# Performance work log

Hardware: AMD Instinct MI355X
Metric: run time of the kernel (lower is better)

Reference implementation:

```python
import jax, jax.numpy as jnp
import numpy as np

L, B, D_IN, D_LAT = 4096, 32, 128, 512

def setup_inputs() -> dict:
    key = jax.random.key(0)
    k1, k2, k3, k4 = jax.random.split(key, 4)
    X = jax.random.normal(k1, (L, B, D_IN), dtype=jnp.float32)
    h = jnp.zeros((B, D_LAT), dtype=jnp.float32)
    wx = jax.random.normal(k2, (D_IN, D_LAT), dtype=jnp.float32)
    wh = jax.random.normal(k3, (D_LAT,), dtype=jnp.float32)
    bh = jax.random.normal(k4, (D_LAT,), dtype=jnp.float32)
    return {"X": X, "h": h, "wx": wx, "wh": wh, "bh": bh}

def reference(X, h, wx, wh, bh):
    # Precompute the input projection for all timesteps (batched matmul outside the scan).
    # U: [L, B, latent]
    U = jnp.einsum('lbi,ij->lbj', X, wx) + bh
    # Linear diagonal recurrence: h_t = h_{t-1} * wh + U_t  (no activation inside loop,
    # matching the torch source which applies tanh only to the collected outputs).
    def step(h_prev, u_t):
        h_t = h_prev * wh + u_t
        return h_t, h_t
    _, hs = jax.lax.scan(step, h, U)  # hs: [L, B, latent]
    return jnp.tanh(hs)
```

## Files before the change

kernel.cpp:

```cpp
#include <hip/hip_runtime.h>
#include <cstdint>
#include <cstddef>

#define L_SEQ 4096
#define BATCH 32
#define DIN 128
#define DLAT 512
#define CHUNK 32
#define NCHUNK (L_SEQ / CHUNK)
#define USTRIDE 522

typedef __attribute__((ext_vector_type(8))) short short8;
typedef __attribute__((ext_vector_type(4))) float f32x4;

__device__ __forceinline__ unsigned short bf16rne(float x) {
    unsigned int b = __builtin_bit_cast(unsigned int, x);
    unsigned int r = b + 0x7FFFu + ((b >> 16) & 1u);
    return (unsigned short)(r >> 16);
}
__device__ __forceinline__ float bf16tof(unsigned short h) {
    return __builtin_bit_cast(float, (unsigned int)h << 16);
}
__device__ __forceinline__ void bf16split3(float x, unsigned short& h,
                                           unsigned short& m, unsigned short& l) {
    h = bf16rne(x);
    float r1 = x - bf16tof(h);
    m = bf16rne(r1);
    float r2 = r1 - bf16tof(m);
    l = bf16rne(r2);
}
__device__ __forceinline__ float pow32(float x) {
    float t = x;
    t = t * t; t = t * t; t = t * t; t = t * t; t = t * t;
    return t;
}

__global__ __launch_bounds__(256) void wx_transform(
    const float* __restrict__ wx,
    unsigned short* __restrict__ wxtH,
    unsigned short* __restrict__ wxtM,
    unsigned short* __restrict__ wxtL)
{
    const int gid  = blockIdx.x * 256 + threadIdx.x;
    const int fid  = gid >> 6;
    const int lane = gid & 63;
    const int kt = fid >> 5, nt = fid & 31;
    const int n  = nt * 16 + (lane & 15);
    const int kb = kt * 32 + (lane >> 4) * 8;

    short8 h8, m8, l8;
#pragma unroll
    for (int i = 0; i < 8; ++i) {
        unsigned short h, m, l;
        bf16split3(wx[(size_t)(kb + i) * DLAT + n], h, m, l);
        h8[i] = (short)h; m8[i] = (short)m; l8[i] = (short)l;
    }
    ((short8*)wxtH)[fid * 64 + lane] = h8;
    ((short8*)wxtM)[fid * 64 + lane] = m8;
    ((short8*)wxtL)[fid * 64 + lane] = l8;
}

__global__ __launch_bounds__(256) void rnn_local_mfma2(
    const float* __restrict__ X,
    const unsigned short* __restrict__ wxtH,
    const unsigned short* __restrict__ wxtM,
    const unsigned short* __restrict__ wxtL,
    const float* __restrict__ wh,
    const float* __restrict__ bh,
    float* __restrict__ out,
    float* __restrict__ F)
{
    __shared__ __align__(16) char smem[16 * 3 * 64 * 8 * 2];
    unsigned short* AF = (unsigned short*)smem;
    float* U = (float*)smem;

    const int tid  = threadIdx.x;
    const int c0 = blockIdx.x * 2, b = blockIdx.y;
    const int wid = tid >> 6, lane = tid & 63;

#pragma unroll
    for (int sl = 0; sl < 4; ++sl) {
        const int slot = tid + sl * 256;
        const int f  = slot >> 6;
        const int ls = slot & 63;
        const int cl = f >> 3, m = (f >> 2) & 1, kt = f & 3;
        const int t  = (c0 + cl) * CHUNK + m * 16 + (ls & 15);
        const int kb = kt * 32 + (ls >> 4) * 8;
        const float* p = X + ((size_t)t * BATCH + b) * DIN + kb;
        const float4 va = *(const float4*)p;
        const float4 vb = *(const float4*)(p + 4);
        float v[8] = {va.x, va.y, va.z, va.w, vb.x, vb.y, vb.z, vb.w};
        short8 h8, m8, l8;
#pragma unroll
        for (int i = 0; i < 8; ++i) {
            unsigned short h, mm, l;
            bf16split3(v[i], h, mm, l);
            h8[i] = (short)h; m8[i] = (short)mm; l8[i] = (short)l;
        }
        ((short8*)AF)[(f * 3 + 0) * 64 + ls] = h8;
        ((short8*)AF)[(f * 3 + 1) * 64 + ls] = m8;
        ((short8*)AF)[(f * 3 + 2) * 64 + ls] = l8;
    }
    __syncthreads();

    f32x4 acc[4][8];
#pragma unroll
    for (int tt = 0; tt < 4; ++tt)
#pragma unroll
        for (int j = 0; j < 8; ++j)
            acc[tt][j] = (f32x4){0.f, 0.f, 0.f, 0.f};

    const short8* AFv = (const short8*)AF;
    const short8* BHp = (const short8*)wxtH;
    const short8* BMp = (const short8*)wxtM;
    const short8* BLp = (const short8*)wxtL;

#pragma unroll
    for (int kt = 0; kt < 4; ++kt) {
        short8 ah[4], am[4], al[4];
#pragma unroll
        for (int tt = 0; tt < 4; ++tt) {
            const int f = tt * 4 + kt;
            ah[tt] = AFv[(f * 3 + 0) * 64 + lane];
            am[tt] = AFv[(f * 3 + 1) * 64 + lane];
            al[tt] = AFv[(f * 3 + 2) * 64 + lane];
        }
#pragma unroll
        for (int j = 0; j < 8; ++j) {
            const int idx = (kt * 32 + wid * 8 + j) * 64 + lane;
            const short8 bh8 = BHp[idx];
            const short8 bm8 = BMp[idx];
            const short8 bl8 = BLp[idx];
#pragma unroll
            for (int tt = 0; tt < 4; ++tt) {
                acc[tt][j] = __builtin_amdgcn_mfma_f32_16x16x32_bf16(am[tt], bm8, acc[tt][j], 0, 0, 0);
                acc[tt][j] = __builtin_amdgcn_mfma_f32_16x16x32_bf16(al[tt], bh8, acc[tt][j], 0, 0, 0);
                acc[tt][j] = __builtin_amdgcn_mfma_f32_16x16x32_bf16(ah[tt], bl8, acc[tt][j], 0, 0, 0);
                acc[tt][j] = __builtin_amdgcn_mfma_f32_16x16x32_bf16(am[tt], bh8, acc[tt][j], 0, 0, 0);
                acc[tt][j] = __builtin_amdgcn_mfma_f32_16x16x32_bf16(ah[tt], bm8, acc[tt][j], 0, 0, 0);
                acc[tt][j] = __builtin_amdgcn_mfma_f32_16x16x32_bf16(ah[tt], bh8, acc[tt][j], 0, 0, 0);
            }
        }
    }

    const int ch = tid * 2;
    const float2 whv = *(const float2*)(wh + ch);
    const float2 bhv = *(const float2*)(bh + ch);
    float l0 = 0.f, l1 = 0.f;

#pragma unroll
    for (int mm = 0; mm < 4; ++mm) {
        const int cl = mm >> 1, m = mm & 1;
        __syncthreads();
#pragma unroll
        for (int j = 0; j < 8; ++j) {
            const int col = wid * 128 + j * 16 + (lane & 15);
#pragma unroll
            for (int r4 = 0; r4 < 4; ++r4)
                U[((lane >> 4) * 4 + r4) * USTRIDE + col] = acc[mm][j][r4];
        }
        __syncthreads();
        for (int tl = 0; tl < 16; ++tl) {
            const float2 u = *(const float2*)&U[tl * USTRIDE + ch];
            l0 = fmaf(l0, whv.x, u.x + bhv.x);
            l1 = fmaf(l1, whv.y, u.y + bhv.y);
            const int t = (c0 + cl) * CHUNK + m * 16 + tl;
            float2 o; o.x = l0; o.y = l1;
            *(float2*)(out + ((size_t)t * BATCH + b) * DLAT + ch) = o;
        }
        if (m == 1) {
            float2 fo; fo.x = l0; fo.y = l1;
            *(float2*)(F + ((size_t)(c0 + cl) * BATCH + b) * DLAT + ch) = fo;
            l0 = 0.f; l1 = 0.f;
        }
    }
}

__global__ __launch_bounds__(128) void rnn_prefix(
    const float* __restrict__ h0, const float* __restrict__ wh,
    const float* __restrict__ F, float* __restrict__ Hpre)
{
    const int b  = blockIdx.x;
    const int j4 = threadIdx.x * 4;
    const size_t cb = (size_t)b * DLAT + j4;
    float4 w4 = *(const float4*)(wh + j4);
    float wv[4] = {w4.x, w4.y, w4.z, w4.w};
    float wc[4];
#pragma unroll
    for (int k = 0; k < 4; ++k) wc[k] = pow32(wv[k]);
    float4 h4 = *(const float4*)(h0 + cb);
    float Hv[4] = {h4.x, h4.y, h4.z, h4.w};
    for (int cg = 0; cg < NCHUNK / 4; ++cg) {
        float4 Fv[4];
#pragma unroll
        for (int i = 0; i < 4; ++i)
            Fv[i] = *(const float4*)(F + (size_t)(cg * 4 + i) * (BATCH * DLAT) + cb);
#pragma unroll
        for (int i = 0; i < 4; ++i) {
            float4 o = {Hv[0], Hv[1], Hv[2], Hv[3]};
            *(float4*)(Hpre + (size_t)(cg * 4 + i) * (BATCH * DLAT) + cb) = o;
            Hv[0] = fmaf(Hv[0], wc[0], Fv[i].x);
            Hv[1] = fmaf(Hv[1], wc[1], Fv[i].y);
            Hv[2] = fmaf(Hv[2], wc[2], Fv[i].z);
            Hv[3] = fmaf(Hv[3], wc[3], Fv[i].w);
        }
    }
}

__global__ __launch_bounds__(256) void rnn_fix2(
    const float* __restrict__ wh, const float* __restrict__ Hpre,
    float* __restrict__ out)
{
    const int tid = threadIdx.x;
    const int c   = blockIdx.x * 2 + (tid >> 7);
    const int b   = blockIdx.y;
    const int j4  = (tid & 127) * 4;
    const size_t cb = (size_t)b * DLAT + j4;
    float4 w4 = *(const float4*)(wh + j4);
    float4 H4 = *(const float4*)(Hpre + (size_t)c * (BATCH * DLAT) + cb);
    float wv[4] = {w4.x, w4.y, w4.z, w4.w};
    float Hv[4] = {H4.x, H4.y, H4.z, H4.w};
    float sc[4] = {wv[0], wv[1], wv[2], wv[3]};
#pragma unroll 4
    for (int d = 0; d < CHUNK; ++d) {
        const size_t off = ((size_t)(c * CHUNK + d) * BATCH + b) * DLAT + j4;
        float4 l4 = *(const float4*)(out + off);
        float4 res;
        res.x = tanhf(fmaf(sc[0], Hv[0], l4.x));
        res.y = tanhf(fmaf(sc[1], Hv[1], l4.y));
        res.z = tanhf(fmaf(sc[2], Hv[2], l4.z));
        res.w = tanhf(fmaf(sc[3], Hv[3], l4.w));
        *(float4*)(out + off) = res;
        sc[0] *= wv[0]; sc[1] *= wv[1]; sc[2] *= wv[2]; sc[3] *= wv[3];
    }
}

__global__ __launch_bounds__(256) void rnn_fix(
    const float* __restrict__ h0, const float* __restrict__ wh,
    const float* __restrict__ F, float* __restrict__ out)
{
    const int tid = threadIdx.x;
    const int c   = blockIdx.x * 2 + (tid >> 7);
    const int b   = blockIdx.y;
    const int j4  = (tid & 127) * 4;
    const size_t cb = (size_t)b * DLAT + j4;
    float4 h4 = *(const float4*)(h0 + cb);
    float4 w4 = *(const float4*)(wh + j4);
    float Hv[4] = {h4.x, h4.y, h4.z, h4.w};
    float wv[4] = {w4.x, w4.y, w4.z, w4.w};
    float wc[4];
#pragma unroll
    for (int k = 0; k < 4; ++k) wc[k] = pow32(wv[k]);
    for (int cc = 0; cc < c; ++cc) {
        const float4 Fv = *(const float4*)(F + ((size_t)cc * BATCH + b) * DLAT + j4);
        Hv[0] = fmaf(Hv[0], wc[0], Fv.x);
        Hv[1] = fmaf(Hv[1], wc[1], Fv.y);
        Hv[2] = fmaf(Hv[2], wc[2], Fv.z);
        Hv[3] = fmaf(Hv[3], wc[3], Fv.w);
    }
    float sc[4] = {wv[0], wv[1], wv[2], wv[3]};
    for (int d = 0; d < CHUNK; ++d) {
        const size_t off = ((size_t)(c * CHUNK + d) * BATCH + b) * DLAT + j4;
        float4 l4 = *(const float4*)(out + off);
        float4 res;
        res.x = tanhf(fmaf(sc[0], Hv[0], l4.x));
        res.y = tanhf(fmaf(sc[1], Hv[1], l4.y));
        res.z = tanhf(fmaf(sc[2], Hv[2], l4.z));
        res.w = tanhf(fmaf(sc[3], Hv[3], l4.w));
        *(float4*)(out + off) = res;
        sc[0] *= wv[0]; sc[1] *= wv[1]; sc[2] *= wv[2]; sc[3] *= wv[3];
    }
}

extern "C" void kernel_launch(void* const* d_in, const int* in_sizes, int n_in,
                              void* d_out, int out_size, void* d_ws, size_t ws_size,
                              hipStream_t stream) {
    const float* X  = (const float*)d_in[0];
    const float* h0 = (const float*)d_in[1];
    const float* wx = (const float*)d_in[2];
    const float* wh = (const float*)d_in[3];
    const float* bh = (const float*)d_in[4];
    float* out = (float*)d_out;

    const size_t seg = (size_t)NCHUNK * BATCH * DLAT;
    const size_t wxt_elems = 4 * 32 * 64 * 8;
    float* F = (float*)d_ws;
    unsigned short* wxtH = (unsigned short*)(F + seg);
    unsigned short* wxtM = wxtH + wxt_elems;
    unsigned short* wxtL = wxtM + wxt_elems;
    float* Hpre = (float*)(wxtL + wxt_elems);

    const size_t need_mid  = seg * 4 + wxt_elems * 3 * 2;
    const size_t need_full = need_mid + seg * 4;

    wx_transform<<<dim3(32), dim3(256), 0, stream>>>(wx, wxtH, wxtM, wxtL);
    rnn_local_mfma2<<<dim3(NCHUNK / 2, BATCH), dim3(256), 0, stream>>>(
        X, wxtH, wxtM, wxtL, wh, bh, out, F);
    if (ws_size >= need_full) {
        rnn_prefix<<<dim3(BATCH), dim3(128), 0, stream>>>(h0, wh, F, Hpre);
        rnn_fix2<<<dim3(NCHUNK / 2, BATCH), dim3(256), 0, stream>>>(wh, Hpre, out);
    } else {
        rnn_fix<<<dim3(NCHUNK / 2, BATCH), dim3(256), 0, stream>>>(h0, wh, F, out);
    }
}
```

Before: 233.1 us.

## Compute in-chunk scan in registers via cross-lane bpermute, one chunk per block

The local kernel now handles one 32-step chunk per block instead of two, which doubles the grid and halves the accumulator registers. The in-chunk linear recurrence is computed directly on the MFMA accumulator layout. Each lane does a 4-step serial scan, then a cross-lane prefix over 16-row groups using ds_bpermute with powers of wh. This removes the LDS round-trip of U, the __syncthreads barriers and the 16-step serial loop per thread. The cost is extra multiplies by wh powers, which can change floating-point rounding, and output stores now scatter across four timestep rows per lane.

```diff
diff --git a/kernel.cpp b/kernel.cpp
--- a/kernel.cpp
+++ b/kernel.cpp
@@ -8,7 +8,6 @@
 #define DLAT 512
 #define CHUNK 32
 #define NCHUNK (L_SEQ / CHUNK)
-#define USTRIDE 522
 
 typedef __attribute__((ext_vector_type(8))) short short8;
 typedef __attribute__((ext_vector_type(4))) float f32x4;
@@ -34,6 +33,10 @@
     t = t * t; t = t * t; t = t * t; t = t * t; t = t * t;
     return t;
 }
+__device__ __forceinline__ float bpermf(int idxb, float v) {
+    return __builtin_bit_cast(float,
+        __builtin_amdgcn_ds_bpermute(idxb, __builtin_bit_cast(int, v)));
+}
 
 __global__ __launch_bounds__(256) void wx_transform(
     const float* __restrict__ wx,
@@ -60,7 +63,7 @@
     ((short8*)wxtL)[fid * 64 + lane] = l8;
 }
 
-__global__ __launch_bounds__(256) void rnn_local_mfma2(
+__global__ __launch_bounds__(256) void rnn_local_mfma3(
     const float* __restrict__ X,
     const unsigned short* __restrict__ wxtH,
     const unsigned short* __restrict__ wxtM,
@@ -70,21 +73,21 @@
     float* __restrict__ out,
     float* __restrict__ F)
 {
-    __shared__ __align__(16) char smem[16 * 3 * 64 * 8 * 2];
-    unsigned short* AF = (unsigned short*)smem;
-    float* U = (float*)smem;
+    __shared__ __align__(16) unsigned short AF[8 * 3 * 64 * 8];
 
     const int tid  = threadIdx.x;
-    const int c0 = blockIdx.x * 2, b = blockIdx.y;
+    const int c = blockIdx.x, b = blockIdx.y;
     const int wid = tid >> 6, lane = tid & 63;
-
-#pragma unroll
-    for (int sl = 0; sl < 4; ++sl) {
+    const int g = lane >> 4;
+    const int col = lane & 15;
+
+#pragma unroll
+    for (int sl = 0; sl < 2; ++sl) {
         const int slot = tid + sl * 256;
         const int f  = slot >> 6;
         const int ls = slot & 63;
-        const int cl = f >> 3, m = (f >> 2) & 1, kt = f & 3;
-        const int t  = (c0 + cl) * CHUNK + m * 16 + (ls & 15);
+        const int mS = f >> 2, kt = f & 3;
+        const int t  = c * CHUNK + mS * 16 + (ls & 15);
         const int kb = kt * 32 + (ls >> 4) * 8;
         const float* p = X + ((size_t)t * BATCH + b) * DIN + kb;
         const float4 va = *(const float4*)p;
@@ -101,14 +104,22 @@
         ((short8*)AF)[(f * 3 + 1) * 64 + ls] = m8;
         ((short8*)AF)[(f * 3 + 2) * 64 + ls] = l8;
     }
+
+    float whj[8], bhj[8];
+#pragma unroll
+    for (int j = 0; j < 8; ++j) {
+        const int chj = wid * 128 + j * 16 + col;
+        whj[j] = wh[chj];
+        bhj[j] = bh[chj];
+    }
     __syncthreads();
 
-    f32x4 acc[4][8];
-#pragma unroll
-    for (int tt = 0; tt < 4; ++tt)
+    f32x4 acc[2][8];
+#pragma unroll
+    for (int m = 0; m < 2; ++m)
 #pragma unroll
         for (int j = 0; j < 8; ++j)
-            acc[tt][j] = (f32x4){0.f, 0.f, 0.f, 0.f};
+            acc[m][j] = (f32x4){0.f, 0.f, 0.f, 0.f};
 
     const short8* AFv = (const short8*)AF;
     const short8* BHp = (const short8*)wxtH;
@@ -117,62 +128,82 @@
 
 #pragma unroll
     for (int kt = 0; kt < 4; ++kt) {
-        short8 ah[4], am[4], al[4];
-#pragma unroll
-        for (int tt = 0; tt < 4; ++tt) {
-            const int f = tt * 4 + kt;
-            ah[tt] = AFv[(f * 3 + 0) * 64 + lane];
-            am[tt] = AFv[(f * 3 + 1) * 64 + lane];
-            al[tt] = AFv[(f * 3 + 2) * 64 + lane];
-        }
+        const short8 a0h = AFv[((0 * 4 + kt) * 3 + 0) * 64 + lane];
+        const short8 a0m = AFv[((0 * 4 + kt) * 3 + 1) * 64 + lane];
+        const short8 a0l = AFv[((0 * 4 + kt) * 3 + 2) * 64 + lane];
+        const short8 a1h = AFv[((1 * 4 + kt) * 3 + 0) * 64 + lane];
+        const short8 a1m = AFv[((1 * 4 + kt) * 3 + 1) * 64 + lane];
+        const short8 a1l = AFv[((1 * 4 + kt) * 3 + 2) * 64 + lane];
 #pragma unroll
         for (int j = 0; j < 8; ++j) {
             const int idx = (kt * 32 + wid * 8 + j) * 64 + lane;
             const short8 bh8 = BHp[idx];
             const short8 bm8 = BMp[idx];
             const short8 bl8 = BLp[idx];
-#pragma unroll
-            for (int tt = 0; tt < 4; ++tt) {
-                acc[tt][j] = __builtin_amdgcn_mfma_f32_16x16x32_bf16(am[tt], bm8, acc[tt][j], 0, 0, 0);
-                acc[tt][j] = __builtin_amdgcn_mfma_f32_16x16x32_bf16(al[tt], bh8, acc[tt][j], 0, 0, 0);
-                acc[tt][j] = __builtin_amdgcn_mfma_f32_16x16x32_bf16(ah[tt], bl8, acc[tt][j], 0, 0, 0);
-                acc[tt][j] = __builtin_amdgcn_mfma_f32_16x16x32_bf16(am[tt], bh8, acc[tt][j], 0, 0, 0);
-                acc[tt][j] = __builtin_amdgcn_mfma_f32_16x16x32_bf16(ah[tt], bm8, acc[tt][j], 0, 0, 0);
-                acc[tt][j] = __builtin_amdgcn_mfma_f32_16x16x32_bf16(ah[tt], bh8, acc[tt][j], 0, 0, 0);
+            acc[0][j] = __builtin_amdgcn_mfma_f32_16x16x32_bf16(a0m, bm8, acc[0][j], 0, 0, 0);
+            acc[0][j] = __builtin_amdgcn_mfma_f32_16x16x32_bf16(a0l, bh8, acc[0][j], 0, 0, 0);
+            acc[0][j] = __builtin_amdgcn_mfma_f32_16x16x32_bf16(a0h, bl8, acc[0][j], 0, 0, 0);
+            acc[0][j] = __builtin_amdgcn_mfma_f32_16x16x32_bf16(a0m, bh8, acc[0][j], 0, 0, 0);
+            acc[0][j] = __builtin_amdgcn_mfma_f32_16x16x32_bf16(a0h, bm8, acc[0][j], 0, 0, 0);
+            acc[0][j] = __builtin_amdgcn_mfma_f32_16x16x32_bf16(a0h, bh8, acc[0][j], 0, 0, 0);
+            acc[1][j] = __builtin_amdgcn_mfma_f32_16x16x32_bf16(a1m, bm8, acc[1][j], 0, 0, 0);
+            acc[1][j] = __builtin_amdgcn_mfma_f32_16x16x32_bf16(a1l, bh8, acc[1][j], 0, 0, 0);
+            acc[1][j] = __builtin_amdgcn_mfma_f32_16x16x32_bf16(a1h, bl8, acc[1][j], 0, 0, 0);
+            acc[1][j] = __builtin_amdgcn_mfma_f32_16x16x32_bf16(a1m, bh8, acc[1][j], 0, 0, 0);
+            acc[1][j] = __builtin_amdgcn_mfma_f32_16x16x32_bf16(a1h, bm8, acc[1][j], 0, 0, 0);
+            acc[1][j] = __builtin_amdgcn_mfma_f32_16x16x32_bf16(a1h, bh8, acc[1][j], 0, 0, 0);
+        }
+    }
+
+    const int i16 = ((lane - 16) & 63) << 2;
+    const int i32 = ((lane - 32) & 63) << 2;
+    const int i48 = (col + 48) << 2;
+    const size_t BD = (size_t)BATCH * DLAT;
+
+#pragma unroll
+    for (int j = 0; j < 8; ++j) {
+        const float w  = whj[j], bb = bhj[j];
+        const float w2 = w * w, w3 = w2 * w, w4 = w2 * w2, w8 = w4 * w4;
+        float h15 = 0.f, hlast = 0.f;
+#pragma unroll
+        for (int m = 0; m < 2; ++m) {
+            const float u0 = acc[m][j][0] + bb;
+            const float u1 = acc[m][j][1] + bb;
+            const float u2 = acc[m][j][2] + bb;
+            const float u3 = acc[m][j][3] + bb;
+            const float p0 = u0;
+            const float p1 = fmaf(p0, w, u1);
+            const float p2 = fmaf(p1, w, u2);
+            const float p3 = fmaf(p2, w, u3);
+            const float t1 = bpermf(i16, p3);
+            const float f1 = (g >= 1) ? fmaf(w4, t1, p3) : p3;
+            const float t2 = bpermf(i32, f1);
+            const float f2 = (g >= 2) ? fmaf(w8, t2, f1) : f1;
+            const float pe = bpermf(i16, f2);
+            float He = (g >= 1) ? pe : 0.0f;
+            if (m == 1) {
+                const float w4g = (g == 0) ? 1.0f : (g == 1) ? w4
+                                 : (g == 2) ? w8 : w4 * w8;
+                He = fmaf(w4g, h15, He);
+            }
+            const float h0v = fmaf(w,  He, p0);
+            const float h1v = fmaf(w2, He, p1);
+            const float h2v = fmaf(w3, He, p2);
+            const float h3v = fmaf(w4, He, p3);
+            const size_t base = ((size_t)(c * CHUNK + m * 16 + g * 4) * BATCH + b) * DLAT
+                                + wid * 128 + j * 16 + col;
+            out[base]          = h0v;
+            out[base + BD]     = h1v;
+            out[base + 2 * BD] = h2v;
+            out[base + 3 * BD] = h3v;
+            if (m == 0) {
+                h15 = bpermf(i48, f2);
+            } else {
+                hlast = h3v;
             }
         }
-    }
-
-    const int ch = tid * 2;
-    const float2 whv = *(const float2*)(wh + ch);
-    const float2 bhv = *(const float2*)(bh + ch);
-    float l0 = 0.f, l1 = 0.f;
-
-#pragma unroll
-    for (int mm = 0; mm < 4; ++mm) {
-        const int cl = mm >> 1, m = mm & 1;
-        __syncthreads();
-#pragma unroll
-        for (int j = 0; j < 8; ++j) {
-            const int col = wid * 128 + j * 16 + (lane & 15);
-#pragma unroll
-            for (int r4 = 0; r4 < 4; ++r4)
-                U[((lane >> 4) * 4 + r4) * USTRIDE + col] = acc[mm][j][r4];
-        }
-        __syncthreads();
-        for (int tl = 0; tl < 16; ++tl) {
-            const float2 u = *(const float2*)&U[tl * USTRIDE + ch];
-            l0 = fmaf(l0, whv.x, u.x + bhv.x);
-            l1 = fmaf(l1, whv.y, u.y + bhv.y);
-            const int t = (c0 + cl) * CHUNK + m * 16 + tl;
-            float2 o; o.x = l0; o.y = l1;
-            *(float2*)(out + ((size_t)t * BATCH + b) * DLAT + ch) = o;
-        }
-        if (m == 1) {
-            float2 fo; fo.x = l0; fo.y = l1;
-            *(float2*)(F + ((size_t)(c0 + cl) * BATCH + b) * DLAT + ch) = fo;
-            l0 = 0.f; l1 = 0.f;
-        }
+        if (g == 3)
+            F[((size_t)c * BATCH + b) * DLAT + wid * 128 + j * 16 + col] = hlast;
     }
 }
 
@@ -290,11 +321,10 @@
     unsigned short* wxtL = wxtM + wxt_elems;
     float* Hpre = (float*)(wxtL + wxt_elems);
 
-    const size_t need_mid  = seg * 4 + wxt_elems * 3 * 2;
-    const size_t need_full = need_mid + seg * 4;
+    const size_t need_full = seg * 4 + wxt_elems * 3 * 2 + seg * 4;
 
     wx_transform<<<dim3(32), dim3(256), 0, stream>>>(wx, wxtH, wxtM, wxtL);
-    rnn_local_mfma2<<<dim3(NCHUNK / 2, BATCH), dim3(256), 0, stream>>>(
+    rnn_local_mfma3<<<dim3(NCHUNK, BATCH), dim3(256), 0, stream>>>(
         X, wxtH, wxtM, wxtL, wh, bh, out, F);
     if (ws_size >= need_full) {
         rnn_prefix<<<dim3(BATCH), dim3(128), 0, stream>>>(h0, wh, F, Hpre);
```

Result: slower. 263.2 us (+12.9%).
